# Optimization experiments

Hardware: AMD Instinct MI355X
Metric: run time of the kernel (lower is better)

The kernel has to match this reference:

```python
import jax, jax.numpy as jnp
import numpy as np

T, H, I, E = 4096, 1024, 512, 16


def setup_inputs() -> dict:
    key = jax.random.key(0)
    k1, k2, k3 = jax.random.split(key, 3)
    x = jax.random.normal(k1, (T, H), dtype=jnp.float32)
    gate_up_proj = jax.random.normal(k2, (E, H, 2 * I), dtype=jnp.float32) * 0.02
    down_proj = jax.random.normal(k3, (E, I, H), dtype=jnp.float32) * 0.02
    # uneven expert token counts summing exactly to T (no padding rows)
    rng = np.random.default_rng(0)
    raw = rng.integers(64, 512, size=E)
    counts = (raw * T) // raw.sum()
    counts[-1] += T - counts.sum()
    num_tokens_per_expert = jnp.asarray(counts, dtype=jnp.int32)
    return {"x": x, "gate_up_proj": gate_up_proj, "down_proj": down_proj,
            "num_tokens_per_expert": num_tokens_per_expert}


def reference(x, gate_up_proj, down_proj, num_tokens_per_expert):
    # tokens are sorted by expert; build per-token expert id (jit-safe: fixed length)
    n_tok = x.shape[0]
    n_exp = gate_up_proj.shape[0]
    seg = jnp.repeat(jnp.arange(n_exp), num_tokens_per_expert, total_repeat_length=n_tok)  # [T]

    def body(acc, ew):
        e, w_gu, w_d = ew
        xe = jnp.where((seg == e)[:, None], x, jnp.zeros((), x.dtype))  # [T, H], zero rows for other experts
        gu = xe @ w_gu                                                  # [T, 2I]
        g, u = jnp.split(gu, 2, axis=-1)
        o = (jax.nn.silu(g) * u) @ w_d                                  # [T, H]; masked rows stay exactly 0
        return acc + o, None

    init = jnp.zeros((n_tok, down_proj.shape[-1]), x.dtype)
    out, _ = jax.lax.scan(body, init, (jnp.arange(n_exp), gate_up_proj, down_proj))
    return out
```

## Files before the change

kernel.cpp:

```cpp
#include <hip/hip_runtime.h>

#define H_DIM 1024
#define I_DIM 512
#define E_EXP 16
#define BM    128
#define BK    64
#define BSTR  68

using bf16x8   = __attribute__((ext_vector_type(8))) short;
using floatx4  = __attribute__((ext_vector_type(4))) float;
using ushort4v = __attribute__((ext_vector_type(4))) unsigned short;

__device__ __forceinline__ unsigned short f2bf(float f) {
  union { float f; unsigned u; } v; v.f = f;
  return (unsigned short)((v.u + 0x7FFFu + ((v.u >> 16) & 1u)) >> 16);
}
__device__ __forceinline__ unsigned pk2(float a, float b) {
  return (unsigned)f2bf(a) | ((unsigned)f2bf(b) << 16);
}

__device__ __forceinline__ void gld16(const void* g, void* l) {
  __builtin_amdgcn_global_load_lds((const __attribute__((address_space(1))) void*)g,
                                   (__attribute__((address_space(3))) void*)l,
                                   16, 0, 0);
}

__device__ __forceinline__ void bar_lgkm() {
  asm volatile("s_waitcnt lgkmcnt(0)" ::: "memory");
  __builtin_amdgcn_sched_barrier(0);
  __builtin_amdgcn_s_barrier();
  __builtin_amdgcn_sched_barrier(0);
}
__device__ __forceinline__ void bar_full() {
  asm volatile("s_waitcnt vmcnt(0) lgkmcnt(0)" ::: "memory");
  __builtin_amdgcn_sched_barrier(0);
  __builtin_amdgcn_s_barrier();
  __builtin_amdgcn_sched_barrier(0);
}

__device__ __forceinline__ bool tile_info(const int* __restrict__ counts, int by,
                                          int& e, int& row0, int& base, int& cnt) {
  int acc = 0, off = 0;
  e = -1;
  #pragma unroll
  for (int i = 0; i < E_EXP; ++i) {
    int c = counts[i];
    int nt = (c + BM - 1) >> 7;
    if (e < 0 && by < acc + nt) { e = i; row0 = (by - acc) * BM; base = off; cnt = c; }
    acc += nt; off += c;
  }
  return e >= 0;
}

__global__ void k_cvt(const float* __restrict__ x, unsigned short* __restrict__ xb) {
  const float4* s4 = (const float4*)x;
  int b0 = blockIdx.x * 512 + threadIdx.x;
  float4 a = s4[b0];
  float4 b = s4[b0 + 256];
  ushort4v oa, ob;
  oa.x = f2bf(a.x); oa.y = f2bf(a.y); oa.z = f2bf(a.z); oa.w = f2bf(a.w);
  ob.x = f2bf(b.x); ob.y = f2bf(b.y); ob.z = f2bf(b.z); ob.w = f2bf(b.w);
  ((ushort4v*)xb)[b0] = oa;
  ((ushort4v*)xb)[b0 + 256] = ob;
}

__launch_bounds__(256, 3)
__global__ void k_gemm_a(const unsigned short* __restrict__ xb,
                         const float* __restrict__ wgu,
                         unsigned short* __restrict__ hb,
                         const int* __restrict__ counts) {
  __shared__ unsigned short As[2][BM * BK];
  __shared__ unsigned short Bs[64 * BSTR];

  int e, row0, base, cnt;
  if (!tile_info(counts, blockIdx.y, e, row0, base, cnt)) return;
  const int rows = (cnt - row0 < BM) ? (cnt - row0) : BM;
  const int c0 = blockIdx.x * 32;

  const int tid = threadIdx.x;
  const int w = tid >> 6, l = tid & 63;
  const int lr = l & 15, q = l >> 4;
  const int asr = l >> 3;
  const int akc = ((l & 7) ^ asr) * 8;
  const int cswz = lr & 7;

  const int f4  = tid & 7;
  const int seg = (tid >> 3) & 1;
  const int kb  = (tid >> 4) * 4;
  const float* gptr = wgu + (size_t)e * H_DIM * (2 * I_DIM) + c0 + f4 * 4 + seg * I_DIM;
  unsigned int* BsD = (unsigned int*)Bs;

  const int mhalf = w & 1, nhalf = w >> 1;
  const int mrow = mhalf * 64;
  const unsigned short* arow = xb + (size_t)(base + row0) * H_DIM;

  int agr[4];
  #pragma unroll
  for (int t = 0; t < 4; ++t) {
    int r = w * 32 + t * 8 + asr;
    agr[t] = (r < rows) ? r : rows - 1;
  }

  floatx4 accg[4], accu[4];
  #pragma unroll
  for (int i = 0; i < 4; ++i) { accg[i] = (floatx4){0,0,0,0}; accu[i] = (floatx4){0,0,0,0}; }

  float4 bv[4];

  auto loadB = [&](int kk) {
    #pragma unroll
    for (int j = 0; j < 4; ++j)
      bv[j] = *(const float4*)&gptr[(size_t)(kk + kb + j) * (2 * I_DIM)];
  };
  auto loadA = [&](int kk, int buf) {
    #pragma unroll
    for (int t = 0; t < 4; ++t)
      gld16(&arow[(size_t)agr[t] * H_DIM + kk + akc], &As[buf][(w * 32 + t * 8) * BK]);
  };
  auto writeB = [&]() {
    #pragma unroll
    for (int c = 0; c < 4; ++c) {
      uint2 d;
      d.x = pk2(bv[0][c], bv[1][c]);
      d.y = pk2(bv[2][c], bv[3][c]);
      *(uint2*)&BsD[(seg * 32 + f4 * 4 + c) * (BSTR / 2) + (kb >> 1)] = d;
    }
  };
  auto compute = [&](int cb) {
    #pragma unroll
    for (int kf = 0; kf < 2; ++kf) {
      const int c = kf * 4 + q;
      const int ca = (c ^ cswz) * 8;
      const int ch = c * 8;
      bf16x8 af[4], bg, bu;
      #pragma unroll
      for (int mi = 0; mi < 4; ++mi)
        af[mi] = *(const bf16x8*)&As[cb][(mrow + mi * 16 + lr) * BK + ca];
      bg = *(const bf16x8*)&Bs[(nhalf * 16 + lr) * BSTR + ch];
      bu = *(const bf16x8*)&Bs[(32 + nhalf * 16 + lr) * BSTR + ch];
      #pragma unroll
      for (int mi = 0; mi < 4; ++mi) {
        accg[mi] = __builtin_amdgcn_mfma_f32_16x16x32_bf16(af[mi], bg, accg[mi], 0, 0, 0);
        accu[mi] = __builtin_amdgcn_mfma_f32_16x16x32_bf16(af[mi], bu, accu[mi], 0, 0, 0);
      }
    }
  };

  loadB(0);
  loadA(0, 0);
  writeB();
  __syncthreads();

  const int nk = H_DIM / BK;
  int cur = 0;
  for (int ki = 0; ki < nk - 1; ++ki) {
    const int kk = (ki + 1) * BK;
    loadB(kk);
    loadA(kk, cur ^ 1);
    __builtin_amdgcn_sched_barrier(0);
    compute(cur);
    bar_lgkm();
    writeB();
    bar_full();
    cur ^= 1;
  }
  compute(cur);

  #pragma unroll
  for (int mi = 0; mi < 4; ++mi)
    #pragma unroll
    for (int r = 0; r < 4; ++r) {
      int row_local = mrow + mi * 16 + q * 4 + r;
      if (row_local >= rows) continue;
      size_t orow = (size_t)(base + row0 + row_local) * I_DIM;
      float g = accg[mi][r], u = accu[mi][r];
      float s = g / (1.0f + __expf(-g)) * u;
      hb[orow + c0 + nhalf * 16 + lr] = f2bf(s);
    }
}

__launch_bounds__(256, 3)
__global__ void k_gemm_b(const unsigned short* __restrict__ hb,
                         const float* __restrict__ wdn,
                         float* __restrict__ out,
                         const int* __restrict__ counts) {
  __shared__ unsigned short As[2][BM * BK];
  __shared__ unsigned short Bs[64 * BSTR];

  int e, row0, base, cnt;
  if (!tile_info(counts, blockIdx.y, e, row0, base, cnt)) return;
  const int rows = (cnt - row0 < BM) ? (cnt - row0) : BM;
  const int n0 = blockIdx.x * 64;

  const int tid = threadIdx.x;
  const int w = tid >> 6, l = tid & 63;
  const int lr = l & 15, q = l >> 4;
  const int asr = l >> 3;
  const int akc = ((l & 7) ^ asr) * 8;
  const int cswz = lr & 7;

  const int f4 = tid & 15;
  const int kb = (tid >> 4) * 4;
  const float* gptr = wdn + (size_t)e * I_DIM * H_DIM + n0 + f4 * 4;
  unsigned int* BsD = (unsigned int*)Bs;

  const int mhalf = w & 1, nhalf = w >> 1;
  const int mrow = mhalf * 64;
  const unsigned short* arow = hb + (size_t)(base + row0) * I_DIM;

  int agr[4];
  #pragma unroll
  for (int t = 0; t < 4; ++t) {
    int r = w * 32 + t * 8 + asr;
    agr[t] = (r < rows) ? r : rows - 1;
  }

  floatx4 acc[4][2];
  #pragma unroll
  for (int i = 0; i < 4; ++i)
    #pragma unroll
    for (int j = 0; j < 2; ++j) acc[i][j] = (floatx4){0,0,0,0};

  float4 bv[4];

  auto loadB = [&](int kk) {
    #pragma unroll
    for (int j = 0; j < 4; ++j)
      bv[j] = *(const float4*)&gptr[(size_t)(kk + kb + j) * H_DIM];
  };
  auto loadA = [&](int kk, int buf) {
    #pragma unroll
    for (int t = 0; t < 4; ++t)
      gld16(&arow[(size_t)agr[t] * I_DIM + kk + akc], &As[buf][(w * 32 + t * 8) * BK]);
  };
  auto writeB = [&]() {
    #pragma unroll
    for (int c = 0; c < 4; ++c) {
      uint2 d;
      d.x = pk2(bv[0][c], bv[1][c]);
      d.y = pk2(bv[2][c], bv[3][c]);
      *(uint2*)&BsD[(f4 * 4 + c) * (BSTR / 2) + (kb >> 1)] = d;
    }
  };
  auto compute = [&](int cb) {
    #pragma unroll
    for (int kf = 0; kf < 2; ++kf) {
      const int c = kf * 4 + q;
      const int ca = (c ^ cswz) * 8;
      const int ch = c * 8;
      bf16x8 af[4], bf[2];
      #pragma unroll
      for (int mi = 0; mi < 4; ++mi)
        af[mi] = *(const bf16x8*)&As[cb][(mrow + mi * 16 + lr) * BK + ca];
      #pragma unroll
      for (int ni = 0; ni < 2; ++ni)
        bf[ni] = *(const bf16x8*)&Bs[(nhalf * 32 + ni * 16 + lr) * BSTR + ch];
      #pragma unroll
      for (int mi = 0; mi < 4; ++mi)
        #pragma unroll
        for (int ni = 0; ni < 2; ++ni)
          acc[mi][ni] = __builtin_amdgcn_mfma_f32_16x16x32_bf16(af[mi], bf[ni], acc[mi][ni], 0, 0, 0);
    }
  };

  loadB(0);
  loadA(0, 0);
  writeB();
  __syncthreads();

  const int nk = I_DIM / BK;
  int cur = 0;
  for (int ki = 0; ki < nk - 1; ++ki) {
    const int kk = (ki + 1) * BK;
    loadB(kk);
    loadA(kk, cur ^ 1);
    __builtin_amdgcn_sched_barrier(0);
    compute(cur);
    bar_lgkm();
    writeB();
    bar_full();
    cur ^= 1;
  }
  compute(cur);

  #pragma unroll
  for (int mi = 0; mi < 4; ++mi)
    #pragma unroll
    for (int r = 0; r < 4; ++r) {
      int row_local = mrow + mi * 16 + q * 4 + r;
      if (row_local >= rows) continue;
      size_t orow = (size_t)(base + row0 + row_local) * H_DIM;
      #pragma unroll
      for (int ni = 0; ni < 2; ++ni)
        out[orow + n0 + nhalf * 32 + ni * 16 + lr] = acc[mi][ni][r];
    }
}

extern "C" void kernel_launch(void* const* d_in, const int* in_sizes, int n_in,
                              void* d_out, int out_size, void* d_ws, size_t ws_size,
                              hipStream_t stream) {
  const float* x      = (const float*)d_in[0];
  const float* wgu    = (const float*)d_in[1];
  const float* wdn    = (const float*)d_in[2];
  const int*   counts = (const int*)d_in[3];
  float* out = (float*)d_out;

  unsigned char* ws = (unsigned char*)d_ws;
  unsigned short* xb = (unsigned short*)(ws);
  unsigned short* hb = (unsigned short*)(ws + 8388608);

  k_cvt<<<2048, 256, 0, stream>>>(x, xb);
  k_gemm_a<<<dim3(I_DIM / 32, 48), 256, 0, stream>>>(xb, wgu, hb, counts);
  k_gemm_b<<<dim3(H_DIM / 64, 48), 256, 0, stream>>>(hb, wdn, out, counts);
}
```

Before: 170.3 us.

## Prefetch B two stages ahead with partial vmcnt waits and remap grid to 1D

The fp32 weight tile loads now run two K-steps ahead in a manually unrolled ping-pong of register buffers. The barrier waits only until the older loads have landed (vmcnt(4)) instead of draining every outstanding global load each step, so weight fetch latency overlaps with more compute. The grid is flattened to 1D with the row tile index varying fastest, so consecutive blocks share the same weight column slice, which may improve L2 reuse of the weights. The cost is higher register pressure from holding two B buffers, and correctness now depends on the ordering of vmcnt counts.

Measured after the change: 171.0 us. Within noise of the previous version (+0.4%).

```diff
diff --git a/kernel.cpp b/kernel.cpp
--- a/kernel.cpp
+++ b/kernel.cpp
@@ -11,6 +11,8 @@
 using floatx4  = __attribute__((ext_vector_type(4))) float;
 using ushort4v = __attribute__((ext_vector_type(4))) unsigned short;
 
+struct BvT { float4 a, b, c, d; };
+
 __device__ __forceinline__ unsigned short f2bf(float f) {
   union { float f; unsigned u; } v; v.f = f;
   return (unsigned short)((v.u + 0x7FFFu + ((v.u >> 16) & 1u)) >> 16);
@@ -31,7 +33,13 @@
   __builtin_amdgcn_s_barrier();
   __builtin_amdgcn_sched_barrier(0);
 }
-__device__ __forceinline__ void bar_full() {
+__device__ __forceinline__ void bar_v4() {
+  asm volatile("s_waitcnt vmcnt(4) lgkmcnt(0)" ::: "memory");
+  __builtin_amdgcn_sched_barrier(0);
+  __builtin_amdgcn_s_barrier();
+  __builtin_amdgcn_sched_barrier(0);
+}
+__device__ __forceinline__ void bar_v0() {
   asm volatile("s_waitcnt vmcnt(0) lgkmcnt(0)" ::: "memory");
   __builtin_amdgcn_sched_barrier(0);
   __builtin_amdgcn_s_barrier();
@@ -64,6 +72,22 @@
   ((ushort4v*)xb)[b0 + 256] = ob;
 }
 
+__device__ __forceinline__ BvT ldB(const float* gptr, int kidx, int rstride) {
+  BvT r;
+  r.a = *(const float4*)&gptr[(size_t)(kidx + 0) * rstride];
+  r.b = *(const float4*)&gptr[(size_t)(kidx + 1) * rstride];
+  r.c = *(const float4*)&gptr[(size_t)(kidx + 2) * rstride];
+  r.d = *(const float4*)&gptr[(size_t)(kidx + 3) * rstride];
+  return r;
+}
+__device__ __forceinline__ void stB(unsigned int* dst, BvT v) {
+  uint2 d;
+  d.x = pk2(v.a.x, v.b.x); d.y = pk2(v.c.x, v.d.x); *(uint2*)&dst[0 * (BSTR/2)] = d;
+  d.x = pk2(v.a.y, v.b.y); d.y = pk2(v.c.y, v.d.y); *(uint2*)&dst[1 * (BSTR/2)] = d;
+  d.x = pk2(v.a.z, v.b.z); d.y = pk2(v.c.z, v.d.z); *(uint2*)&dst[2 * (BSTR/2)] = d;
+  d.x = pk2(v.a.w, v.b.w); d.y = pk2(v.c.w, v.d.w); *(uint2*)&dst[3 * (BSTR/2)] = d;
+}
+
 __launch_bounds__(256, 3)
 __global__ void k_gemm_a(const unsigned short* __restrict__ xb,
                          const float* __restrict__ wgu,
@@ -72,10 +96,12 @@
   __shared__ unsigned short As[2][BM * BK];
   __shared__ unsigned short Bs[64 * BSTR];
 
+  const int gid = blockIdx.x;
+  const int by = gid % 48, bx = gid / 48;
   int e, row0, base, cnt;
-  if (!tile_info(counts, blockIdx.y, e, row0, base, cnt)) return;
+  if (!tile_info(counts, by, e, row0, base, cnt)) return;
   const int rows = (cnt - row0 < BM) ? (cnt - row0) : BM;
-  const int c0 = blockIdx.x * 32;
+  const int c0 = bx * 32;
 
   const int tid = threadIdx.x;
   const int w = tid >> 6, l = tid & 63;
@@ -88,43 +114,30 @@
   const int seg = (tid >> 3) & 1;
   const int kb  = (tid >> 4) * 4;
   const float* gptr = wgu + (size_t)e * H_DIM * (2 * I_DIM) + c0 + f4 * 4 + seg * I_DIM;
-  unsigned int* BsD = (unsigned int*)Bs;
+  unsigned int* bsd = (unsigned int*)Bs + (seg * 32 + f4 * 4) * (BSTR / 2) + (kb >> 1);
 
   const int mhalf = w & 1, nhalf = w >> 1;
   const int mrow = mhalf * 64;
   const unsigned short* arow = xb + (size_t)(base + row0) * H_DIM;
 
-  int agr[4];
-  #pragma unroll
-  for (int t = 0; t < 4; ++t) {
-    int r = w * 32 + t * 8 + asr;
-    agr[t] = (r < rows) ? r : rows - 1;
+  int agr0, agr1, agr2, agr3;
+  {
+    int r0 = w * 32 + asr,      r1 = r0 + 8, r2 = r0 + 16, r3 = r0 + 24;
+    agr0 = (r0 < rows) ? r0 : rows - 1;
+    agr1 = (r1 < rows) ? r1 : rows - 1;
+    agr2 = (r2 < rows) ? r2 : rows - 1;
+    agr3 = (r3 < rows) ? r3 : rows - 1;
   }
 
   floatx4 accg[4], accu[4];
   #pragma unroll
   for (int i = 0; i < 4; ++i) { accg[i] = (floatx4){0,0,0,0}; accu[i] = (floatx4){0,0,0,0}; }
 
-  float4 bv[4];
-
-  auto loadB = [&](int kk) {
-    #pragma unroll
-    for (int j = 0; j < 4; ++j)
-      bv[j] = *(const float4*)&gptr[(size_t)(kk + kb + j) * (2 * I_DIM)];
-  };
   auto loadA = [&](int kk, int buf) {
-    #pragma unroll
-    for (int t = 0; t < 4; ++t)
-      gld16(&arow[(size_t)agr[t] * H_DIM + kk + akc], &As[buf][(w * 32 + t * 8) * BK]);
-  };
-  auto writeB = [&]() {
-    #pragma unroll
-    for (int c = 0; c < 4; ++c) {
-      uint2 d;
-      d.x = pk2(bv[0][c], bv[1][c]);
-      d.y = pk2(bv[2][c], bv[3][c]);
-      *(uint2*)&BsD[(seg * 32 + f4 * 4 + c) * (BSTR / 2) + (kb >> 1)] = d;
-    }
+    gld16(&arow[(size_t)agr0 * H_DIM + kk + akc], &As[buf][(w * 32 +  0) * BK]);
+    gld16(&arow[(size_t)agr1 * H_DIM + kk + akc], &As[buf][(w * 32 +  8) * BK]);
+    gld16(&arow[(size_t)agr2 * H_DIM + kk + akc], &As[buf][(w * 32 + 16) * BK]);
+    gld16(&arow[(size_t)agr3 * H_DIM + kk + akc], &As[buf][(w * 32 + 24) * BK]);
   };
   auto compute = [&](int cb) {
     #pragma unroll
@@ -146,24 +159,42 @@
     }
   };
 
-  loadB(0);
+  BvT b0 = ldB(gptr, 0 * BK + kb, 2 * I_DIM);
   loadA(0, 0);
-  writeB();
-  __syncthreads();
-
-  const int nk = H_DIM / BK;
+  BvT b1 = ldB(gptr, 1 * BK + kb, 2 * I_DIM);
+  stB(bsd, b0);
+  bar_v4();
   int cur = 0;
-  for (int ki = 0; ki < nk - 1; ++ki) {
-    const int kk = (ki + 1) * BK;
-    loadB(kk);
-    loadA(kk, cur ^ 1);
+
+  #pragma unroll 1
+  for (int i = 0; i < 7; ++i) {
+    const int s = 2 * i;
+    loadA((s + 1) * BK, cur ^ 1);
+    __builtin_amdgcn_sched_barrier(0);
+    b0 = ldB(gptr, (s + 2) * BK + kb, 2 * I_DIM);
     __builtin_amdgcn_sched_barrier(0);
     compute(cur);
     bar_lgkm();
-    writeB();
-    bar_full();
+    stB(bsd, b1);
+    bar_v4();
     cur ^= 1;
-  }
+    loadA((s + 2) * BK, cur ^ 1);
+    __builtin_amdgcn_sched_barrier(0);
+    b1 = ldB(gptr, (s + 3) * BK + kb, 2 * I_DIM);
+    __builtin_amdgcn_sched_barrier(0);
+    compute(cur);
+    bar_lgkm();
+    stB(bsd, b0);
+    bar_v4();
+    cur ^= 1;
+  }
+  loadA(15 * BK, cur ^ 1);
+  __builtin_amdgcn_sched_barrier(0);
+  compute(cur);
+  bar_lgkm();
+  stB(bsd, b1);
+  bar_v0();
+  cur ^= 1;
   compute(cur);
 
   #pragma unroll
@@ -187,10 +218,12 @@
   __shared__ unsigned short As[2][BM * BK];
   __shared__ unsigned short Bs[64 * BSTR];
 
+  const int gid = blockIdx.x;
+  const int by = gid % 48, bx = gid / 48;
   int e, row0, base, cnt;
-  if (!tile_info(counts, blockIdx.y, e, row0, base, cnt)) return;
+  if (!tile_info(counts, by, e, row0, base, cnt)) return;
   const int rows = (cnt - row0 < BM) ? (cnt - row0) : BM;
-  const int n0 = blockIdx.x * 64;
+  const int n0 = bx * 64;
 
   const int tid = threadIdx.x;
   const int w = tid >> 6, l = tid & 63;
@@ -202,17 +235,19 @@
   const int f4 = tid & 15;
   const int kb = (tid >> 4) * 4;
   const float* gptr = wdn + (size_t)e * I_DIM * H_DIM + n0 + f4 * 4;
-  unsigned int* BsD = (unsigned int*)Bs;
+  unsigned int* bsd = (unsigned int*)Bs + (f4 * 4) * (BSTR / 2) + (kb >> 1);
 
   const int mhalf = w & 1, nhalf = w >> 1;
   const int mrow = mhalf * 64;
   const unsigned short* arow = hb + (size_t)(base + row0) * I_DIM;
 
-  int agr[4];
-  #pragma unroll
-  for (int t = 0; t < 4; ++t) {
-    int r = w * 32 + t * 8 + asr;
-    agr[t] = (r < rows) ? r : rows - 1;
+  int agr0, agr1, agr2, agr3;
+  {
+    int r0 = w * 32 + asr,      r1 = r0 + 8, r2 = r0 + 16, r3 = r0 + 24;
+    agr0 = (r0 < rows) ? r0 : rows - 1;
+    agr1 = (r1 < rows) ? r1 : rows - 1;
+    agr2 = (r2 < rows) ? r2 : rows - 1;
+    agr3 = (r3 < rows) ? r3 : rows - 1;
   }
 
   floatx4 acc[4][2];
@@ -221,26 +256,11 @@
     #pragma unroll
     for (int j = 0; j < 2; ++j) acc[i][j] = (floatx4){0,0,0,0};
 
-  float4 bv[4];
-
-  auto loadB = [&](int kk) {
-    #pragma unroll
-    for (int j = 0; j < 4; ++j)
-      bv[j] = *(const float4*)&gptr[(size_t)(kk + kb + j) * H_DIM];
-  };
   auto loadA = [&](int kk, int buf) {
-    #pragma unroll
-    for (int t = 0; t < 4; ++t)
-      gld16(&arow[(size_t)agr[t] * I_DIM + kk + akc], &As[buf][(w * 32 + t * 8) * BK]);
-  };
-  auto writeB = [&]() {
-    #pragma unroll
-    for (int c = 0; c < 4; ++c) {
-      uint2 d;
-      d.x = pk2(bv[0][c], bv[1][c]);
-      d.y = pk2(bv[2][c], bv[3][c]);
-      *(uint2*)&BsD[(f4 * 4 + c) * (BSTR / 2) + (kb >> 1)] = d;
-    }
+    gld16(&arow[(size_t)agr0 * I_DIM + kk + akc], &As[buf][(w * 32 +  0) * BK]);
+    gld16(&arow[(size_t)agr1 * I_DIM + kk + akc], &As[buf][(w * 32 +  8) * BK]);
+    gld16(&arow[(size_t)agr2 * I_DIM + kk + akc], &As[buf][(w * 32 + 16) * BK]);
+    gld16(&arow[(size_t)agr3 * I_DIM + kk + akc], &As[buf][(w * 32 + 24) * BK]);
   };
   auto compute = [&](int cb) {
     #pragma unroll
@@ -263,24 +283,42 @@
     }
   };
 
-  loadB(0);
+  BvT b0 = ldB(gptr, 0 * BK + kb, H_DIM);
   loadA(0, 0);
-  writeB();
-  __syncthreads();
-
-  const int nk = I_DIM / BK;
+  BvT b1 = ldB(gptr, 1 * BK + kb, H_DIM);
+  stB(bsd, b0);
+  bar_v4();
   int cur = 0;
-  for (int ki = 0; ki < nk - 1; ++ki) {
-    const int kk = (ki + 1) * BK;
-    loadB(kk);
-    loadA(kk, cur ^ 1);
+
+  #pragma unroll 1
+  for (int i = 0; i < 3; ++i) {
+    const int s = 2 * i;
+    loadA((s + 1) * BK, cur ^ 1);
+    __builtin_amdgcn_sched_barrier(0);
+    b0 = ldB(gptr, (s + 2) * BK + kb, H_DIM);
     __builtin_amdgcn_sched_barrier(0);
     compute(cur);
     bar_lgkm();
-    writeB();
-    bar_full();
+    stB(bsd, b1);
+    bar_v4();
     cur ^= 1;
-  }
+    loadA((s + 2) * BK, cur ^ 1);
+    __builtin_amdgcn_sched_barrier(0);
+    b1 = ldB(gptr, (s + 3) * BK + kb, H_DIM);
+    __builtin_amdgcn_sched_barrier(0);
+    compute(cur);
+    bar_lgkm();
+    stB(bsd, b0);
+    bar_v4();
+    cur ^= 1;
+  }
+  loadA(7 * BK, cur ^ 1);
+  __builtin_amdgcn_sched_barrier(0);
+  compute(cur);
+  bar_lgkm();
+  stB(bsd, b1);
+  bar_v0();
+  cur ^= 1;
   compute(cur);
 
   #pragma unroll
@@ -310,6 +348,6 @@
   unsigned short* hb = (unsigned short*)(ws + 8388608);
 
   k_cvt<<<2048, 256, 0, stream>>>(x, xb);
-  k_gemm_a<<<dim3(I_DIM / 32, 48), 256, 0, stream>>>(xb, wgu, hb, counts);
-  k_gemm_b<<<dim3(H_DIM / 64, 48), 256, 0, stream>>>(hb, wdn, out, counts);
-}
+  k_gemm_a<<<768, 256, 0, stream>>>(xb, wgu, hb, counts);
+  k_gemm_b<<<768, 256, 0, stream>>>(hb, wdn, out, counts);
+}
```
